# Kernel tuning notes

Hardware: AMD Instinct MI355X
Metric: run time of the kernel (lower is better)

Reference implementation:

```python
import jax, jax.numpy as jnp
import numpy as np

H = 32   # rnn_hidden_dim * num_directions
L = 2    # num_layers
F = 1    # num_features
B, T = 2048, 1024


def _xavier(key, shape):
    lim = np.sqrt(6.0 / (shape[0] + shape[1])).astype(np.float32)
    return jax.random.uniform(key, shape, jnp.float32, -lim, lim)


def _lstm_uniform(key, shape):
    lim = np.float32(1.0 / np.sqrt(H))
    return jax.random.uniform(key, shape, jnp.float32, -lim, lim)


def setup_inputs() -> dict:
    key = jax.random.key(0)
    ks = jax.random.split(key, 12)
    return {
        "padded_sequence": jax.random.normal(ks[0], (B, T, F), jnp.float32),
        "z": jax.random.normal(ks[1], (B, H), jnp.float32),
        "lengths": jnp.full((B,), T, jnp.int32),
        # LSTM layer 0 (input size F)
        "w_ih0": _lstm_uniform(ks[2], (4 * H, F)),
        "w_hh0": _lstm_uniform(ks[3], (4 * H, H)),
        "b_ih0": _lstm_uniform(ks[4], (4 * H,)).reshape(4 * H),
        "b_hh0": _lstm_uniform(ks[5], (4 * H,)).reshape(4 * H),
        # LSTM layer 1 (input size H)
        "w_ih1": _lstm_uniform(ks[6], (4 * H, H)),
        "w_hh1": _lstm_uniform(ks[7], (4 * H, H)),
        "b_ih1": _lstm_uniform(ks[8], (4 * H,)).reshape(4 * H),
        "b_hh1": _lstm_uniform(ks[9], (4 * H,)).reshape(4 * H),
        # output projection (xavier weight, bias filled 0.01 per _init_weights)
        "w_out": _xavier(ks[10], (F, H)),
        "b_out": jnp.full((F,), 0.01, jnp.float32),
    }


def _cell(x, h, c, w_ih, w_hh, b):
    # PyTorch LSTM gate order: i, f, g, o
    gates = x @ w_ih.T + h @ w_hh.T + b  # (B, 4H)
    i, f, g, o = jnp.split(gates, 4, axis=-1)
    c_new = jax.nn.sigmoid(f) * c + jax.nn.sigmoid(i) * jnp.tanh(g)
    h_new = jax.nn.sigmoid(o) * jnp.tanh(c_new)
    return h_new, c_new


def reference(padded_sequence, z, lengths, w_ih0, w_hh0, b_ih0, b_hh0,
              w_ih1, w_hh1, b_ih1, b_hh1, w_out, b_out):
    b_sz, n_steps, f = padded_sequence.shape
    b0 = b_ih0 + b_hh0
    b1 = b_ih1 + b_hh1
    pred0 = jnp.zeros((b_sz, f), padded_sequence.dtype)
    # hidden = (z.repeat(L,1,1), z.repeat(L,1,1)): both layers' h and c start as z
    init = (pred0, z, z, z, z)

    def step(carry, _):
        pred, h0, c0, h1, c1 = carry
        h0n, c0n = _cell(pred, h0, c0, w_ih0, w_hh0, b0)
        h1n, c1n = _cell(h0n, h1, c1, w_ih1, w_hh1, b1)
        pred_n = h1n @ w_out.T + b_out  # (B, F)
        return (pred_n, h0n, c0n, h1n, c1n), pred_n

    _, preds = jax.lax.scan(step, init, None, length=n_steps)  # (T, B, F)
    recovered = jnp.transpose(preds, (1, 0, 2))  # (B, T, F)
    loss = jnp.mean((padded_sequence - recovered) ** 2)
    return loss, recovered
```

## Files before the change

### kernel.cpp

```cpp
#include <hip/hip_runtime.h>

#define NB 2048
#define NT 1024

typedef _Float16 half2_t __attribute__((ext_vector_type(2)));
union F4H { float4 f; half2_t h[4]; };

__device__ __forceinline__ float sig_fast(float x) {
    return __builtin_amdgcn_rcpf(1.0f + __builtin_amdgcn_exp2f(-1.4426950408889634f * x));
}
__device__ __forceinline__ float tanh_fast(float x) {
    return fmaf(2.0f, __builtin_amdgcn_rcpf(1.0f + __builtin_amdgcn_exp2f(-2.8853900817779268f * x)), -1.0f);
}

__global__ void zero_loss_kernel(float* out) { out[0] = 0.0f; }

#define LD4(P, i) (*(const float4*)&(P)[i])
#define FDOT(acc, w, hh) acc = __builtin_amdgcn_fdot2((w), (hh), (acc), false)
#define PINH(v) asm volatile("" : "+v"(v))

#define CVTQ(n0, n1, p, i) { float4 r_ = LD4(p, i); \
  n0.x=(_Float16)r_.x; n0.y=(_Float16)r_.y; n1.x=(_Float16)r_.z; n1.y=(_Float16)r_.w; }

#define DECL_ROWH(n, src, row) \
  half2_t n##0,n##1,n##2,n##3,n##4,n##5,n##6,n##7,n##8,n##9,n##10,n##11,n##12,n##13,n##14,n##15; \
  CVTQ(n##0, n##1, src,(row)*32+ 0) CVTQ(n##2, n##3, src,(row)*32+ 4) \
  CVTQ(n##4, n##5, src,(row)*32+ 8) CVTQ(n##6, n##7, src,(row)*32+12) \
  CVTQ(n##8, n##9, src,(row)*32+16) CVTQ(n##10,n##11,src,(row)*32+20) \
  CVTQ(n##12,n##13,src,(row)*32+24) CVTQ(n##14,n##15,src,(row)*32+28) \
  PINH(n##0); PINH(n##1); PINH(n##2); PINH(n##3); PINH(n##4); PINH(n##5); PINH(n##6); PINH(n##7); \
  PINH(n##8); PINH(n##9); PINH(n##10); PINH(n##11); PINH(n##12); PINH(n##13); PINH(n##14); PINH(n##15);

#define DOT4(aa, ab, wA0,wA1,wA2,wA3, wB0,wB1,wB2,wB3, U) \
  FDOT(aa, wA0, (U).h[0]); FDOT(ab, wB0, (U).h[0]); \
  FDOT(aa, wA1, (U).h[1]); FDOT(ab, wB1, (U).h[1]); \
  FDOT(aa, wA2, (U).h[2]); FDOT(ab, wB2, (U).h[2]); \
  FDOT(aa, wA3, (U).h[3]); FDOT(ab, wB3, (U).h[3]);

__global__ __launch_bounds__(64) __attribute__((amdgpu_waves_per_eu(1, 2)))
void decoder_lstm_kernel(const float* __restrict__ seq,
                         const float* __restrict__ z,
                         const float* __restrict__ w_ih0,
                         const float* __restrict__ w_hh0,
                         const float* __restrict__ b_ih0,
                         const float* __restrict__ b_hh0,
                         const float* __restrict__ w_ih1,
                         const float* __restrict__ w_hh1,
                         const float* __restrict__ b_ih1,
                         const float* __restrict__ b_hh1,
                         const float* __restrict__ w_out,
                         const float* __restrict__ b_out,
                         float* __restrict__ out)
{
    const int b  = blockIdx.x;
    const int l  = threadIdx.x;
    const int lo = l & 31;

    __shared__ float4 sh0f[8];
    __shared__ float4 sh1f[8];
    _Float16* sh0h = (_Float16*)sh0f;
    _Float16* sh1h = (_Float16*)sh1f;

    const int rA = l;
    const int rB = l + 64;

    const float wih0A  = w_ih0[rA];
    const float wih0B  = w_ih0[rB];
    const float bias0A = b_ih0[rA] + b_hh0[rA];
    const float bias0B = b_ih0[rB] + b_hh0[rB];
    const float bias1A = b_ih1[rA] + b_hh1[rA];
    const float bias1B = b_ih1[rB] + b_hh1[rB];

    const float m    = (l < 32) ? 1.0f : 0.0f;
    const float wOut = (l < 32) ? w_out[lo] : 0.0f;
    const float bOut = b_out[0];

    DECL_ROWH(w0A, w_hh0, rA)
    DECL_ROWH(w0B, w_hh0, rB)
    DECL_ROWH(wiA, w_ih1, rA)
    DECL_ROWH(wiB, w_ih1, rB)
    DECL_ROWH(whA, w_hh1, rA)
    DECL_ROWH(whB, w_hh1, rB)

    float zv = z[(size_t)b * 32 + lo];
    float cc0 = zv, cc1 = zv;
    sh0h[l] = (_Float16)zv;
    sh1h[l] = (_Float16)zv;
    float pred = 0.0f, sse = 0.0f, xreg = 0.0f;

    const float* seq_b = seq + (size_t)b * NT;
    float* out_b = out + 1 + (size_t)b * NT;

    __builtin_amdgcn_wave_barrier();

    for (int t = 0; t < NT; ++t) {
        if ((t & 63) == 0) xreg = seq_b[t + l];

        F4H U0, U1, U2, U3, X0, X1, X2, X3;
        U0.f = sh0f[0]; U1.f = sh0f[1]; U2.f = sh0f[2]; U3.f = sh0f[3];
        X0.f = sh1f[0]; X1.f = sh1f[1]; X2.f = sh1f[2]; X3.f = sh1f[3];

        float a0 = fmaf(pred, wih0A, bias0A), a1 = 0.0f;
        float b0 = fmaf(pred, wih0B, bias0B), b1 = 0.0f;
        DOT4(a0, b0, w0A0,w0A1,w0A2,w0A3,     w0B0,w0B1,w0B2,w0B3,     U0);
        DOT4(a1, b1, w0A4,w0A5,w0A6,w0A7,     w0B4,w0B5,w0B6,w0B7,     U1);
        DOT4(a0, b0, w0A8,w0A9,w0A10,w0A11,   w0B8,w0B9,w0B10,w0B11,   U2);
        DOT4(a1, b1, w0A12,w0A13,w0A14,w0A15, w0B12,w0B13,w0B14,w0B15, U3);
        float gA = a0 + a1;
        float gB = b0 + b1;

        float sA  = sig_fast(gA);
        float gBx = fmaf(m, gB, gB);
        float sB  = sig_fast(gBx);
        float vB  = fmaf(m, sB - 1.0f, sB);

        float fOrI = __shfl_xor(sA, 32);
        float oOrG = __shfl_xor(vB, 32);
        cc0 = fmaf(fOrI, cc0, sA * vB);
        float h0n = oOrG * tanh_fast(cc0);
        sh0h[l] = (_Float16)h0n;
        __builtin_amdgcn_wave_barrier();

        F4H V0, V1, V2, V3;
        V0.f = sh0f[0]; V1.f = sh0f[1]; V2.f = sh0f[2]; V3.f = sh0f[3];
        float cA0 = bias1A, cA1 = 0.0f;
        float cB0 = bias1B, cB1 = 0.0f;
        DOT4(cA0, cB0, wiA0,wiA1,wiA2,wiA3,     wiB0,wiB1,wiB2,wiB3,     V0);
        DOT4(cA1, cB1, wiA4,wiA5,wiA6,wiA7,     wiB4,wiB5,wiB6,wiB7,     V1);
        DOT4(cA0, cB0, wiA8,wiA9,wiA10,wiA11,   wiB8,wiB9,wiB10,wiB11,   V2);
        DOT4(cA1, cB1, wiA12,wiA13,wiA14,wiA15, wiB12,wiB13,wiB14,wiB15, V3);
        DOT4(cA0, cB0, whA0,whA1,whA2,whA3,     whB0,whB1,whB2,whB3,     X0);
        DOT4(cA1, cB1, whA4,whA5,whA6,whA7,     whB4,whB5,whB6,whB7,     X1);
        DOT4(cA0, cB0, whA8,whA9,whA10,whA11,   whB8,whB9,whB10,whB11,   X2);
        DOT4(cA1, cB1, whA12,whA13,whA14,whA15, whB12,whB13,whB14,whB15, X3);
        float g1A = cA0 + cA1;
        float g1B = cB0 + cB1;

        float s1A  = sig_fast(g1A);
        float g1Bx = fmaf(m, g1B, g1B);
        float s1B  = sig_fast(g1Bx);
        float v1B  = fmaf(m, s1B - 1.0f, s1B);

        float f1 = __shfl_xor(s1A, 32);
        float o1 = __shfl_xor(v1B, 32);
        cc1 = fmaf(f1, cc1, s1A * v1B);
        float h1n = o1 * tanh_fast(cc1);
        sh1h[l] = (_Float16)h1n;

        float term = wOut * h1n;
        term += __shfl_xor(term, 1);
        term += __shfl_xor(term, 2);
        term += __shfl_xor(term, 4);
        term += __shfl_xor(term, 8);
        term += __shfl_xor(term, 16);
        term += __shfl_xor(term, 32);
        pred = term + bOut;
        __builtin_amdgcn_wave_barrier();

        out_b[t] = pred;
        float d    = xreg - pred;
        float dsel = ((t & 63) == l) ? d : 0.0f;
        sse = fmaf(dsel, d, sse);
    }

    sse += __shfl_xor(sse, 1);
    sse += __shfl_xor(sse, 2);
    sse += __shfl_xor(sse, 4);
    sse += __shfl_xor(sse, 8);
    sse += __shfl_xor(sse, 16);
    sse += __shfl_xor(sse, 32);
    if (l == 0) {
        atomicAdd(out, sse * (1.0f / ((float)NB * (float)NT)));
    }
}

extern "C" void kernel_launch(void* const* d_in, const int* in_sizes, int n_in,
                              void* d_out, int out_size, void* d_ws, size_t ws_size,
                              hipStream_t stream) {
    const float* seq   = (const float*)d_in[0];
    const float* z     = (const float*)d_in[1];
    const float* w_ih0 = (const float*)d_in[3];
    const float* w_hh0 = (const float*)d_in[4];
    const float* b_ih0 = (const float*)d_in[5];
    const float* b_hh0 = (const float*)d_in[6];
    const float* w_ih1 = (const float*)d_in[7];
    const float* w_hh1 = (const float*)d_in[8];
    const float* b_ih1 = (const float*)d_in[9];
    const float* b_hh1 = (const float*)d_in[10];
    const float* w_out = (const float*)d_in[11];
    const float* b_out = (const float*)d_in[12];
    float* out = (float*)d_out;

    hipLaunchKernelGGL(zero_loss_kernel, dim3(1), dim3(1), 0, stream, out);
    hipLaunchKernelGGL(decoder_lstm_kernel, dim3(NB), dim3(64), 0, stream,
                       seq, z, w_ih0, w_hh0, b_ih0, b_hh0,
                       w_ih1, w_hh1, b_ih1, b_hh1, w_out, b_out, out);
}
```

Before: 946.3 us.

## Split each sequence's LSTM gates across two waves, one gate row per lane

Each batch element now runs on a 128-thread block of two waves, and each lane computes one gate row instead of two. This halves the per-thread dot-product chain and the weight registers per lane. Hidden states are double-buffered in shared memory, and the output projection is reduced partly across waves through shared memory. The cost is two block-wide __syncthreads per timestep in place of cheap wave barriers, plus cross-wave latency on the serial recurrence.

```diff
diff --git a/kernel.cpp b/kernel.cpp
--- a/kernel.cpp
+++ b/kernel.cpp
@@ -31,13 +31,17 @@
   PINH(n##0); PINH(n##1); PINH(n##2); PINH(n##3); PINH(n##4); PINH(n##5); PINH(n##6); PINH(n##7); \
   PINH(n##8); PINH(n##9); PINH(n##10); PINH(n##11); PINH(n##12); PINH(n##13); PINH(n##14); PINH(n##15);
 
-#define DOT4(aa, ab, wA0,wA1,wA2,wA3, wB0,wB1,wB2,wB3, U) \
-  FDOT(aa, wA0, (U).h[0]); FDOT(ab, wB0, (U).h[0]); \
-  FDOT(aa, wA1, (U).h[1]); FDOT(ab, wB1, (U).h[1]); \
-  FDOT(aa, wA2, (U).h[2]); FDOT(ab, wB2, (U).h[2]); \
-  FDOT(aa, wA3, (U).h[3]); FDOT(ab, wB3, (U).h[3]);
+#define DOT16(a0, a1, n, U0, U1, U2, U3) \
+  FDOT(a0, n##0,  (U0).h[0]); FDOT(a1, n##1,  (U0).h[1]); \
+  FDOT(a0, n##2,  (U0).h[2]); FDOT(a1, n##3,  (U0).h[3]); \
+  FDOT(a0, n##4,  (U1).h[0]); FDOT(a1, n##5,  (U1).h[1]); \
+  FDOT(a0, n##6,  (U1).h[2]); FDOT(a1, n##7,  (U1).h[3]); \
+  FDOT(a0, n##8,  (U2).h[0]); FDOT(a1, n##9,  (U2).h[1]); \
+  FDOT(a0, n##10, (U2).h[2]); FDOT(a1, n##11, (U2).h[3]); \
+  FDOT(a0, n##12, (U3).h[0]); FDOT(a1, n##13, (U3).h[1]); \
+  FDOT(a0, n##14, (U3).h[2]); FDOT(a1, n##15, (U3).h[3]);
 
-__global__ __launch_bounds__(64) __attribute__((amdgpu_waves_per_eu(1, 2)))
+__global__ __launch_bounds__(128)
 void decoder_lstm_kernel(const float* __restrict__ seq,
                          const float* __restrict__ z,
                          const float* __restrict__ w_ih0,
@@ -52,125 +56,113 @@
                          const float* __restrict__ b_out,
                          float* __restrict__ out)
 {
-    const int b  = blockIdx.x;
-    const int l  = threadIdx.x;
-    const int lo = l & 31;
+    const int tid = threadIdx.x;
+    const int w   = tid >> 6;
+    const int l   = tid & 63;
+    const int q   = l >> 4;
+    const int u   = 16 * w + (l & 15);
+    const int R   = q * 32 + u;
+    const int b   = blockIdx.x;
 
-    __shared__ float4 sh0f[8];
-    __shared__ float4 sh1f[8];
-    _Float16* sh0h = (_Float16*)sh0f;
-    _Float16* sh1h = (_Float16*)sh1f;
+    __shared__ __align__(16) _Float16 h0buf[2][32];
+    __shared__ __align__(16) _Float16 h1buf[2][32];
+    __shared__ float pb[2];
 
-    const int rA = l;
-    const int rB = l + 64;
+    DECL_ROWH(w0, w_hh0, R)
+    DECL_ROWH(wi, w_ih1, R)
+    DECL_ROWH(wh, w_hh1, R)
 
-    const float wih0A  = w_ih0[rA];
-    const float wih0B  = w_ih0[rB];
-    const float bias0A = b_ih0[rA] + b_hh0[rA];
-    const float bias0B = b_ih0[rB] + b_hh0[rB];
-    const float bias1A = b_ih1[rA] + b_hh1[rA];
-    const float bias1B = b_ih1[rB] + b_hh1[rB];
+    const float wih0R = w_ih0[R];
+    const float bias0 = b_ih0[R] + b_hh0[R];
+    const float bias1 = b_ih1[R] + b_hh1[R];
 
-    const float m    = (l < 32) ? 1.0f : 0.0f;
-    const float wOut = (l < 32) ? w_out[lo] : 0.0f;
-    const float bOut = b_out[0];
+    const float m2 = (q == 2) ? 1.0f : 0.0f;
+    const float eM = (q == 2) ? -2.8853900817779268f : -1.4426950408889634f;
 
-    DECL_ROWH(w0A, w_hh0, rA)
-    DECL_ROWH(w0B, w_hh0, rB)
-    DECL_ROWH(wiA, w_ih1, rA)
-    DECL_ROWH(wiB, w_ih1, rB)
-    DECL_ROWH(whA, w_hh1, rA)
-    DECL_ROWH(whB, w_hh1, rB)
+    const float wOutL = (l < 16) ? w_out[u] : 0.0f;
+    const float bOut  = b_out[0];
 
-    float zv = z[(size_t)b * 32 + lo];
-    float cc0 = zv, cc1 = zv;
-    sh0h[l] = (_Float16)zv;
-    sh1h[l] = (_Float16)zv;
+    const float cz = z[(size_t)b * 32 + u];
+    float c0 = cz, c1 = cz;
+    if (l < 16) { h0buf[0][u] = (_Float16)cz; h1buf[0][u] = (_Float16)cz; }
     float pred = 0.0f, sse = 0.0f, xreg = 0.0f;
 
     const float* seq_b = seq + (size_t)b * NT;
     float* out_b = out + 1 + (size_t)b * NT;
 
-    __builtin_amdgcn_wave_barrier();
+    __syncthreads();
 
     for (int t = 0; t < NT; ++t) {
-        if ((t & 63) == 0) xreg = seq_b[t + l];
+        const int par = t & 1;
+        if (w == 0 && (t & 63) == 0) xreg = seq_b[t + l];
 
         F4H U0, U1, U2, U3, X0, X1, X2, X3;
-        U0.f = sh0f[0]; U1.f = sh0f[1]; U2.f = sh0f[2]; U3.f = sh0f[3];
-        X0.f = sh1f[0]; X1.f = sh1f[1]; X2.f = sh1f[2]; X3.f = sh1f[3];
+        {
+            const float4* p0 = (const float4*)h0buf[par];
+            const float4* p1 = (const float4*)h1buf[par];
+            U0.f = p0[0]; U1.f = p0[1]; U2.f = p0[2]; U3.f = p0[3];
+            X0.f = p1[0]; X1.f = p1[1]; X2.f = p1[2]; X3.f = p1[3];
+        }
 
-        float a0 = fmaf(pred, wih0A, bias0A), a1 = 0.0f;
-        float b0 = fmaf(pred, wih0B, bias0B), b1 = 0.0f;
-        DOT4(a0, b0, w0A0,w0A1,w0A2,w0A3,     w0B0,w0B1,w0B2,w0B3,     U0);
-        DOT4(a1, b1, w0A4,w0A5,w0A6,w0A7,     w0B4,w0B5,w0B6,w0B7,     U1);
-        DOT4(a0, b0, w0A8,w0A9,w0A10,w0A11,   w0B8,w0B9,w0B10,w0B11,   U2);
-        DOT4(a1, b1, w0A12,w0A13,w0A14,w0A15, w0B12,w0B13,w0B14,w0B15, U3);
-        float gA = a0 + a1;
-        float gB = b0 + b1;
+        float a0 = fmaf(pred, wih0R, bias0), a1 = 0.0f;
+        DOT16(a0, a1, w0, U0, U1, U2, U3);
+        float v  = a0 + a1;
+        float s  = __builtin_amdgcn_rcpf(1.0f + __builtin_amdgcn_exp2f(eM * v));
+        float av = fmaf(m2, s - 1.0f, s);
 
-        float sA  = sig_fast(gA);
-        float gBx = fmaf(m, gB, gB);
-        float sB  = sig_fast(gBx);
-        float vB  = fmaf(m, sB - 1.0f, sB);
-
-        float fOrI = __shfl_xor(sA, 32);
-        float oOrG = __shfl_xor(vB, 32);
-        cc0 = fmaf(fOrI, cc0, sA * vB);
-        float h0n = oOrG * tanh_fast(cc0);
-        sh0h[l] = (_Float16)h0n;
-        __builtin_amdgcn_wave_barrier();
+        float x16 = __shfl_xor(av, 16);
+        float x32 = __shfl_xor(av, 32);
+        float x48 = __shfl_xor(av, 48);
+        c0 = fmaf(x16, c0, av * x32);
+        float h0n = x48 * tanh_fast(c0);
+        if (l < 16) h0buf[par ^ 1][u] = (_Float16)h0n;
+        __syncthreads();
 
         F4H V0, V1, V2, V3;
-        V0.f = sh0f[0]; V1.f = sh0f[1]; V2.f = sh0f[2]; V3.f = sh0f[3];
-        float cA0 = bias1A, cA1 = 0.0f;
-        float cB0 = bias1B, cB1 = 0.0f;
-        DOT4(cA0, cB0, wiA0,wiA1,wiA2,wiA3,     wiB0,wiB1,wiB2,wiB3,     V0);
-        DOT4(cA1, cB1, wiA4,wiA5,wiA6,wiA7,     wiB4,wiB5,wiB6,wiB7,     V1);
-        DOT4(cA0, cB0, wiA8,wiA9,wiA10,wiA11,   wiB8,wiB9,wiB10,wiB11,   V2);
-        DOT4(cA1, cB1, wiA12,wiA13,wiA14,wiA15, wiB12,wiB13,wiB14,wiB15, V3);
-        DOT4(cA0, cB0, whA0,whA1,whA2,whA3,     whB0,whB1,whB2,whB3,     X0);
-        DOT4(cA1, cB1, whA4,whA5,whA6,whA7,     whB4,whB5,whB6,whB7,     X1);
-        DOT4(cA0, cB0, whA8,whA9,whA10,whA11,   whB8,whB9,whB10,whB11,   X2);
-        DOT4(cA1, cB1, whA12,whA13,whA14,whA15, whB12,whB13,whB14,whB15, X3);
-        float g1A = cA0 + cA1;
-        float g1B = cB0 + cB1;
+        {
+            const float4* p = (const float4*)h0buf[par ^ 1];
+            V0.f = p[0]; V1.f = p[1]; V2.f = p[2]; V3.f = p[3];
+        }
+        float d0 = bias1, d1 = 0.0f, d2 = 0.0f, d3 = 0.0f;
+        DOT16(d0, d1, wi, V0, V1, V2, V3);
+        DOT16(d2, d3, wh, X0, X1, X2, X3);
+        float v1  = (d0 + d1) + (d2 + d3);
+        float s1  = __builtin_amdgcn_rcpf(1.0f + __builtin_amdgcn_exp2f(eM * v1));
+        float av1 = fmaf(m2, s1 - 1.0f, s1);
 
-        float s1A  = sig_fast(g1A);
-        float g1Bx = fmaf(m, g1B, g1B);
-        float s1B  = sig_fast(g1Bx);
-        float v1B  = fmaf(m, s1B - 1.0f, s1B);
+        float y16 = __shfl_xor(av1, 16);
+        float y32 = __shfl_xor(av1, 32);
+        float y48 = __shfl_xor(av1, 48);
+        c1 = fmaf(y16, c1, av1 * y32);
+        float h1n = y48 * tanh_fast(c1);
+        if (l < 16) h1buf[par ^ 1][u] = (_Float16)h1n;
 
-        float f1 = __shfl_xor(s1A, 32);
-        float o1 = __shfl_xor(v1B, 32);
-        cc1 = fmaf(f1, cc1, s1A * v1B);
-        float h1n = o1 * tanh_fast(cc1);
-        sh1h[l] = (_Float16)h1n;
-
-        float term = wOut * h1n;
+        float term = wOutL * h1n;
         term += __shfl_xor(term, 1);
         term += __shfl_xor(term, 2);
         term += __shfl_xor(term, 4);
         term += __shfl_xor(term, 8);
-        term += __shfl_xor(term, 16);
-        term += __shfl_xor(term, 32);
-        pred = term + bOut;
-        __builtin_amdgcn_wave_barrier();
+        if (l == 0) pb[w] = term;
+        __syncthreads();
 
-        out_b[t] = pred;
-        float d    = xreg - pred;
-        float dsel = ((t & 63) == l) ? d : 0.0f;
-        sse = fmaf(dsel, d, sse);
+        pred = bOut + pb[0] + pb[1];
+
+        if (w == 0) {
+            out_b[t] = pred;
+            float d    = xreg - pred;
+            float dsel = ((t & 63) == l) ? d : 0.0f;
+            sse = fmaf(dsel, d, sse);
+        }
     }
 
-    sse += __shfl_xor(sse, 1);
-    sse += __shfl_xor(sse, 2);
-    sse += __shfl_xor(sse, 4);
-    sse += __shfl_xor(sse, 8);
-    sse += __shfl_xor(sse, 16);
-    sse += __shfl_xor(sse, 32);
-    if (l == 0) {
-        atomicAdd(out, sse * (1.0f / ((float)NB * (float)NT)));
+    if (w == 0) {
+        sse += __shfl_xor(sse, 1);
+        sse += __shfl_xor(sse, 2);
+        sse += __shfl_xor(sse, 4);
+        sse += __shfl_xor(sse, 8);
+        sse += __shfl_xor(sse, 16);
+        sse += __shfl_xor(sse, 32);
+        if (l == 0) atomicAdd(out, sse * (1.0f / ((float)NB * (float)NT)));
     }
 }
 
@@ -192,7 +184,7 @@
     float* out = (float*)d_out;
 
     hipLaunchKernelGGL(zero_loss_kernel, dim3(1), dim3(1), 0, stream, out);
-    hipLaunchKernelGGL(decoder_lstm_kernel, dim3(NB), dim3(64), 0, stream,
+    hipLaunchKernelGGL(decoder_lstm_kernel, dim3(NB), dim3(128), 0, stream,
                        seq, z, w_ih0, w_hh0, b_ih0, b_hh0,
                        w_ih1, w_hh1, b_ih1, b_hh1, w_out, b_out, out);
 }
```

After: 1.149 ms. +21.5%, slower.
